# Kernel optimization log

Measured on AMD Instinct MI355X. Metric: run time of the kernel, lower is better.

The kernel has to match this reference:

```python
import jax, jax.numpy as jnp
import numpy as np

B, A, C = 1, 196416, 90
H = W = 1024
SCORE_THRESHOLD = 0.05
MAX_DETECTIONS = 100
# RetinaNet-style BBoxTransform normalization (mean=0, std=[0.1,0.1,0.2,0.2])
STD = (0.1, 0.1, 0.2, 0.2)


def setup_inputs() -> dict:
    key = jax.random.key(0)
    k1, k2, k3, k4, k5, k6, k7 = jax.random.split(key, 7)
    x = jax.random.normal(k1, (B, 3, H, W), dtype=jnp.float32)
    regression = jax.random.normal(k2, (B, A, 4), dtype=jnp.float32) * 0.1
    classification = jax.random.normal(k3, (B, A, C), dtype=jnp.float32)
    # valid anchor boxes (x1, y1, x2, y2)
    cx = jax.random.uniform(k4, (B, A), minval=0.0, maxval=float(W))
    cy = jax.random.uniform(k5, (B, A), minval=0.0, maxval=float(H))
    aw = jax.random.uniform(k6, (B, A), minval=16.0, maxval=256.0)
    ah = jax.random.uniform(k7, (B, A), minval=16.0, maxval=256.0)
    anchors = jnp.stack([cx - 0.5 * aw, cy - 0.5 * ah, cx + 0.5 * aw, cy + 0.5 * ah], axis=2).astype(jnp.float32)
    return {"x": x, "regression": regression, "classification": classification, "anchors": anchors}


def _decode_clip(anchors, regression, img_h, img_w):
    # BBoxTransform: deltas (dx, dy, dw, dh) scaled by std, applied to anchor center/size
    wa = anchors[..., 2] - anchors[..., 0]
    ha = anchors[..., 3] - anchors[..., 1]
    cxa = anchors[..., 0] + 0.5 * wa
    cya = anchors[..., 1] + 0.5 * ha
    dx = regression[..., 0] * STD[0]
    dy = regression[..., 1] * STD[1]
    dw = regression[..., 2] * STD[2]
    dh = regression[..., 3] * STD[3]
    cx = cxa + dx * wa
    cy = cya + dy * ha
    w = jnp.exp(dw) * wa
    h = jnp.exp(dh) * ha
    # ClipBoxes: x1,y1 clamped at 0; x2,y2 clamped at image width/height
    x1 = jnp.maximum(cx - 0.5 * w, 0.0)
    y1 = jnp.maximum(cy - 0.5 * h, 0.0)
    x2 = jnp.minimum(cx + 0.5 * w, float(img_w))
    y2 = jnp.minimum(cy + 0.5 * h, float(img_h))
    return jnp.stack([x1, y1, x2, y2], axis=2)  # [B, A, 4]


def reference(x, regression, classification, anchors):
    img_h, img_w = x.shape[2], x.shape[3]
    boxes = _decode_clip(anchors, regression, img_h, img_w)  # [1, A, 4]
    probs = jax.nn.sigmoid(classification)                    # [1, A, C]
    scores = jnp.max(probs, axis=2)                           # [1, A]
    classes = jnp.argmax(probs, axis=2)                       # [1, A]
    valid_scores = jnp.where(scores > SCORE_THRESHOLD, scores, 0.0)
    vb = boxes[0]            # [A, 4]
    vc = classes[0]          # [A]
    vs = valid_scores[0]     # [A]
    k = min(MAX_DETECTIONS, vs.shape[0])
    _, top_idx = jax.lax.top_k(vs, k)
    final_boxes = vb[top_idx]
    final_scores = vs[top_idx]
    final_classes = vc[top_idx]
    return (final_boxes, final_scores, final_classes)
```

## Files before the change

### kernel.cpp

```cpp
#include <hip/hip_runtime.h>
#include <cmath>

#define A_CNT 196416
#define C_CNT 90
#define PAIRS (A_CNT / 2)
#define TOPK 100u
#define RB 128
#define NB_REDUCE ((PAIRS + RB - 1) / RB)

#define OFF_HIST1 785664u
#define OFF_HIST2 789760u
#define OFF_CTRL  1051904u
#define OFF_CAND  1051968u
#define OFF_EQ    1052480u

__global__ __launch_bounds__(RB) void k_reduce(const float* __restrict__ cls,
                                               unsigned* __restrict__ keys,
                                               unsigned* __restrict__ hist1,
                                               unsigned* __restrict__ hist2) {
    __shared__ unsigned lhist[576];
    const int t = threadIdx.x;
    for (int j = t; j < 576; j += RB) lhist[j] = 0u;
    __syncthreads();

    const int p = blockIdx.x * RB + t;
    if (p < PAIRS) {
        const float4* __restrict__ r4 = (const float4*)cls + (size_t)p * 45;
        float m0 = -INFINITY, m1;
#pragma unroll
        for (int i = 0; i < 22; ++i) {
            float4 v = r4[i];
            m0 = fmaxf(m0, fmaxf(fmaxf(v.x, v.y), fmaxf(v.z, v.w)));
        }
        {
            float4 v = r4[22];
            m0 = fmaxf(m0, fmaxf(v.x, v.y));
            m1 = fmaxf(v.z, v.w);
        }
#pragma unroll
        for (int i = 23; i < 45; ++i) {
            float4 v = r4[i];
            m1 = fmaxf(m1, fmaxf(fmaxf(v.x, v.y), fmaxf(v.z, v.w)));
        }
        float p0 = 1.0f / (1.0f + expf(-m0));
        float p1 = 1.0f / (1.0f + expf(-m1));
        unsigned k0 = (p0 > 0.05f) ? __float_as_uint(p0) : 0u;
        unsigned k1 = (p1 > 0.05f) ? __float_as_uint(p1) : 0u;
        *(uint2*)(keys + 2 * p) = make_uint2(k0, k1);
        unsigned h0 = k0 ? (min(k0 >> 16, 0x3F80u) - 0x3D4Bu) : 0u;
        unsigned h1 = k1 ? (min(k1 >> 16, 0x3F80u) - 0x3D4Bu) : 0u;
        atomicAdd(&lhist[h0], 1u);
        atomicAdd(&lhist[h1], 1u);
        if (p < 65536) hist2[p] = 0u;
    }
    __syncthreads();
    for (int j = t; j < 576; j += RB) {
        unsigned c = lhist[j];
        if (c) atomicAdd(&hist1[j], c);
    }
}

template <int CHUNK>
__global__ __launch_bounds__(256) void k_scan(const unsigned* __restrict__ hist,
                                              unsigned* __restrict__ ctrl, int mode) {
    __shared__ unsigned sdata[256];
    __shared__ unsigned sbin[2];
    const int t = threadIdx.x;
    const unsigned target = TOPK;
    const unsigned above0 = (mode == 0) ? 0u : ctrl[1];

    unsigned s = 0;
    const uint4* p = (const uint4*)(hist + t * CHUNK);
#pragma unroll 8
    for (int j = 0; j < CHUNK / 4; ++j) { uint4 u = p[j]; s += u.x + u.y + u.z + u.w; }
    sdata[t] = s;
    for (int d = 1; d < 256; d <<= 1) {
        __syncthreads();
        unsigned add = (t + d < 256) ? sdata[t + d] : 0u;
        __syncthreads();
        sdata[t] += add;
    }
    __syncthreads();
    {
        unsigned mysuf  = sdata[t] + above0;
        unsigned nxtsuf = ((t < 255) ? sdata[t + 1] : 0u) + above0;
        if (nxtsuf < target && mysuf >= target) { sbin[0] = (unsigned)t; sbin[1] = nxtsuf - above0; }
    }
    __syncthreads();
    const unsigned chunkB = sbin[0];
    const unsigned gAbove = sbin[1] + above0;

    unsigned v = (t < CHUNK) ? hist[chunkB * CHUNK + t] : 0u;
    sdata[t] = v;
    for (int d = 1; d < 256; d <<= 1) {
        __syncthreads();
        unsigned add = (t + d < 256) ? sdata[t + d] : 0u;
        __syncthreads();
        sdata[t] += add;
    }
    __syncthreads();
    {
        unsigned mysuf  = sdata[t] + gAbove;
        unsigned nxtsuf = ((t < 255) ? sdata[t + 1] : 0u) + gAbove;
        if (nxtsuf < target && mysuf >= target) {
            unsigned bin = chunkB * CHUNK + (unsigned)t;
            if (mode == 0) {
                ctrl[0] = bin ? (bin + 0x3D4Bu) : 0u;
                ctrl[1] = nxtsuf;
            } else {
                ctrl[2] = (ctrl[0] << 16) | bin;
                ctrl[3] = nxtsuf;
                ctrl[4] = target - nxtsuf;
            }
        }
    }
}

__global__ __launch_bounds__(256) void k_hist2(const unsigned* __restrict__ keys,
                                               const unsigned* __restrict__ ctrl,
                                               unsigned* __restrict__ hist2) {
    const unsigned binB = ctrl[0];
    const int i4 = blockIdx.x * 256 + threadIdx.x;
    if (i4 >= A_CNT / 4) return;
    uint4 k = ((const uint4*)keys)[i4];
    if ((k.x >> 16) == binB) atomicAdd(&hist2[k.x & 0xFFFFu], 1u);
    if ((k.y >> 16) == binB) atomicAdd(&hist2[k.y & 0xFFFFu], 1u);
    if ((k.z >> 16) == binB) atomicAdd(&hist2[k.z & 0xFFFFu], 1u);
    if ((k.w >> 16) == binB) atomicAdd(&hist2[k.w & 0xFFFFu], 1u);
}

__global__ __launch_bounds__(256) void k_gather(const unsigned* __restrict__ keys,
                                                unsigned* __restrict__ ctrl,
                                                unsigned* __restrict__ cand,
                                                unsigned* __restrict__ eqi) {
    const unsigned T = ctrl[2];
    const int i4 = blockIdx.x * 256 + threadIdx.x;
    if (i4 >= A_CNT / 4) return;
    uint4 k = ((const uint4*)keys)[i4];
    const unsigned base = (unsigned)(4 * i4);
#pragma unroll
    for (int j = 0; j < 4; ++j) {
        unsigned kk = (j == 0) ? k.x : (j == 1) ? k.y : (j == 2) ? k.z : k.w;
        if (kk > T) {
            unsigned q = atomicAdd(&ctrl[5], 1u);
            if (q < 128u) cand[q] = base + j;
        } else if (kk == T) {
            unsigned q = atomicAdd(&ctrl[6], 1u);
            if (q < 1024u) eqi[q] = base + j;
        }
    }
}

__global__ __launch_bounds__(128) void k_final(const float* __restrict__ cls,
                                               const float* __restrict__ reg,
                                               const float* __restrict__ anc,
                                               const unsigned* __restrict__ ctrl,
                                               const unsigned* __restrict__ cand,
                                               const unsigned* __restrict__ eqi,
                                               const unsigned* __restrict__ keys,
                                               float* __restrict__ out) {
    __shared__ unsigned sel[TOPK];
    const int t = threadIdx.x;
    const unsigned n_gt = ctrl[3];
    const unsigned need_eq = ctrl[4];
    unsigned eq_cnt = ctrl[6];
    if (eq_cnt > 1024u) eq_cnt = 1024u;

    if (t < (int)n_gt) {
        unsigned mi = cand[t], mk = keys[mi], r = 0;
        for (unsigned j = 0; j < n_gt; ++j) {
            unsigned oj = cand[j], ok = keys[oj];
            if (ok > mk || (ok == mk && oj < mi)) r++;
        }
        sel[r] = mi;
    }
    for (unsigned e = (unsigned)t; e < eq_cnt; e += 128u) {
        unsigned mi = eqi[e], r = 0;
        for (unsigned j = 0; j < eq_cnt; ++j)
            if (eqi[j] < mi) r++;
        if (r < need_eq) sel[n_gt + r] = mi;
    }
    __syncthreads();

    if (t < (int)TOPK) {
        const unsigned a = sel[t];
        const float2* row = (const float2*)(cls + (size_t)a * C_CNT);
        float bv = -INFINITY; int bi = 0;
#pragma unroll 5
        for (int c = 0; c < 45; ++c) {
            float2 v = row[c];
            if (v.x > bv) { bv = v.x; bi = 2 * c; }
            if (v.y > bv) { bv = v.y; bi = 2 * c + 1; }
        }
        float score = __uint_as_float(keys[a]);
        float x1a = anc[a * 4 + 0], y1a = anc[a * 4 + 1];
        float x2a = anc[a * 4 + 2], y2a = anc[a * 4 + 3];
        float wa = x2a - x1a, ha = y2a - y1a;
        float cxa = x1a + 0.5f * wa, cya = y1a + 0.5f * ha;
        float dx = reg[a * 4 + 0] * 0.1f, dy = reg[a * 4 + 1] * 0.1f;
        float dw = reg[a * 4 + 2] * 0.2f, dh = reg[a * 4 + 3] * 0.2f;
        float cx = cxa + dx * wa, cy = cya + dy * ha;
        float w = expf(dw) * wa, h = expf(dh) * ha;
        out[t * 4 + 0] = fmaxf(cx - 0.5f * w, 0.0f);
        out[t * 4 + 1] = fmaxf(cy - 0.5f * h, 0.0f);
        out[t * 4 + 2] = fminf(cx + 0.5f * w, 1024.0f);
        out[t * 4 + 3] = fminf(cy + 0.5f * h, 1024.0f);
        out[400 + t] = score;
        out[500 + t] = (float)bi;
    }
}

extern "C" void kernel_launch(void* const* d_in, const int* in_sizes, int n_in,
                              void* d_out, int out_size, void* d_ws, size_t ws_size,
                              hipStream_t stream) {
    const float* reg = (const float*)d_in[1];
    const float* cls = (const float*)d_in[2];
    const float* anc = (const float*)d_in[3];
    float* out = (float*)d_out;
    char* ws = (char*)d_ws;
    unsigned* keys  = (unsigned*)ws;
    unsigned* hist1 = (unsigned*)(ws + OFF_HIST1);
    unsigned* hist2 = (unsigned*)(ws + OFF_HIST2);
    unsigned* ctrl  = (unsigned*)(ws + OFF_CTRL);
    unsigned* cand  = (unsigned*)(ws + OFF_CAND);
    unsigned* eqi   = (unsigned*)(ws + OFF_EQ);

    hipMemsetAsync(hist1, 0, 1024 * 4, stream);
    hipMemsetAsync(ctrl, 0, 64, stream);
    k_reduce<<<NB_REDUCE, RB, 0, stream>>>(cls, keys, hist1, hist2);
    k_scan<4><<<1, 256, 0, stream>>>(hist1, ctrl, 0);
    k_hist2<<<192, 256, 0, stream>>>(keys, ctrl, hist2);
    k_scan<256><<<1, 256, 0, stream>>>(hist2, ctrl, 1);
    k_gather<<<192, 256, 0, stream>>>(keys, ctrl, cand, eqi);
    k_final<<<1, 128, 0, stream>>>(cls, reg, anc, ctrl, cand, eqi, keys, out);
}
```

Baseline: 165.8 us.

## Coalesce class-max reduction across lanes and drop second radix histogram pass

The reduction kernel now assigns 8 lanes to each anchor pair, so every row of class scores is read with strided float4 loads across lanes and combined by shuffle instead of one thread reading 180 floats serially. This targets poor coalescing and low memory-level parallelism in the dominant read of the classification tensor. It also drops the 16-bit second histogram and its scan; all keys in the threshold bin (up to 2048) are gathered and ranked in shared memory inside the final kernel. That removes two launches and a hist2 clear, at the cost of an O(n^2) ranking over the bin candidates in a single block, and keys beyond the 2048-entry buffer are silently dropped.

```diff
diff --git a/kernel.cpp b/kernel.cpp
--- a/kernel.cpp
+++ b/kernel.cpp
@@ -4,75 +4,78 @@
 #define A_CNT 196416
 #define C_CNT 90
 #define PAIRS (A_CNT / 2)
+#define WITERS 12276
 #define TOPK 100u
-#define RB 128
-#define NB_REDUCE ((PAIRS + RB - 1) / RB)
+#define CAPB 2048
 
 #define OFF_HIST1 785664u
-#define OFF_HIST2 789760u
-#define OFF_CTRL  1051904u
-#define OFF_CAND  1051968u
-#define OFF_EQ    1052480u
-
-__global__ __launch_bounds__(RB) void k_reduce(const float* __restrict__ cls,
-                                               unsigned* __restrict__ keys,
-                                               unsigned* __restrict__ hist1,
-                                               unsigned* __restrict__ hist2) {
+#define OFF_CTRL  789760u
+#define OFF_CANDA 789824u
+#define OFF_CANDB 790336u
+
+__global__ __launch_bounds__(256, 4) void k_reduce(const float* __restrict__ cls,
+                                                   unsigned* __restrict__ keys,
+                                                   unsigned* __restrict__ hist1) {
     __shared__ unsigned lhist[576];
     const int t = threadIdx.x;
-    for (int j = t; j < 576; j += RB) lhist[j] = 0u;
-    __syncthreads();
-
-    const int p = blockIdx.x * RB + t;
-    if (p < PAIRS) {
-        const float4* __restrict__ r4 = (const float4*)cls + (size_t)p * 45;
-        float m0 = -INFINITY, m1;
+    for (int j = t; j < 576; j += 256) lhist[j] = 0u;
+    __syncthreads();
+
+    const int lane = t & 63;
+    const int g = lane >> 3, s = lane & 7;
+    const int wid = blockIdx.x * 4 + (t >> 6);
+    const int nw = gridDim.x * 4;
+    const float4* __restrict__ cls4 = (const float4*)cls;
+
+    for (int w = wid; w < WITERS; w += nw) {
+        const int p = w * 8 + g;
+        const float4* __restrict__ r4 = cls4 + (size_t)p * 45;
+        float m0 = -INFINITY, m1 = -INFINITY;
 #pragma unroll
-        for (int i = 0; i < 22; ++i) {
-            float4 v = r4[i];
-            m0 = fmaxf(m0, fmaxf(fmaxf(v.x, v.y), fmaxf(v.z, v.w)));
-        }
-        {
-            float4 v = r4[22];
-            m0 = fmaxf(m0, fmaxf(v.x, v.y));
-            m1 = fmaxf(v.z, v.w);
+        for (int i = 0; i < 6; ++i) {
+            const int j = s + 8 * i;
+            if (j < 45) {
+                float4 v = r4[j];
+                float a01 = fmaxf(v.x, v.y), a23 = fmaxf(v.z, v.w);
+                float all = fmaxf(a01, a23);
+                if (j < 22)      m0 = fmaxf(m0, all);
+                else if (j > 22) m1 = fmaxf(m1, all);
+                else { m0 = fmaxf(m0, a01); m1 = fmaxf(m1, a23); }
+            }
         }
 #pragma unroll
-        for (int i = 23; i < 45; ++i) {
-            float4 v = r4[i];
-            m1 = fmaxf(m1, fmaxf(fmaxf(v.x, v.y), fmaxf(v.z, v.w)));
-        }
-        float p0 = 1.0f / (1.0f + expf(-m0));
-        float p1 = 1.0f / (1.0f + expf(-m1));
-        unsigned k0 = (p0 > 0.05f) ? __float_as_uint(p0) : 0u;
-        unsigned k1 = (p1 > 0.05f) ? __float_as_uint(p1) : 0u;
-        *(uint2*)(keys + 2 * p) = make_uint2(k0, k1);
-        unsigned h0 = k0 ? (min(k0 >> 16, 0x3F80u) - 0x3D4Bu) : 0u;
-        unsigned h1 = k1 ? (min(k1 >> 16, 0x3F80u) - 0x3D4Bu) : 0u;
-        atomicAdd(&lhist[h0], 1u);
-        atomicAdd(&lhist[h1], 1u);
-        if (p < 65536) hist2[p] = 0u;
-    }
-    __syncthreads();
-    for (int j = t; j < 576; j += RB) {
+        for (int d = 1; d < 8; d <<= 1) {
+            m0 = fmaxf(m0, __shfl_xor(m0, d));
+            m1 = fmaxf(m1, __shfl_xor(m1, d));
+        }
+        if (s == 0) {
+            float p0 = 1.0f / (1.0f + expf(-m0));
+            float p1 = 1.0f / (1.0f + expf(-m1));
+            unsigned k0 = (p0 > 0.05f) ? __float_as_uint(p0) : 0u;
+            unsigned k1 = (p1 > 0.05f) ? __float_as_uint(p1) : 0u;
+            *(uint2*)(keys + 2 * p) = make_uint2(k0, k1);
+            unsigned h0 = k0 ? (min(k0 >> 16, 0x3F80u) - 0x3D4Bu) : 0u;
+            unsigned h1 = k1 ? (min(k1 >> 16, 0x3F80u) - 0x3D4Bu) : 0u;
+            atomicAdd(&lhist[h0], 1u);
+            atomicAdd(&lhist[h1], 1u);
+        }
+    }
+    __syncthreads();
+    for (int j = t; j < 576; j += 256) {
         unsigned c = lhist[j];
         if (c) atomicAdd(&hist1[j], c);
     }
 }
 
-template <int CHUNK>
 __global__ __launch_bounds__(256) void k_scan(const unsigned* __restrict__ hist,
-                                              unsigned* __restrict__ ctrl, int mode) {
+                                              unsigned* __restrict__ ctrl) {
     __shared__ unsigned sdata[256];
     __shared__ unsigned sbin[2];
     const int t = threadIdx.x;
     const unsigned target = TOPK;
-    const unsigned above0 = (mode == 0) ? 0u : ctrl[1];
-
-    unsigned s = 0;
-    const uint4* p = (const uint4*)(hist + t * CHUNK);
-#pragma unroll 8
-    for (int j = 0; j < CHUNK / 4; ++j) { uint4 u = p[j]; s += u.x + u.y + u.z + u.w; }
+
+    uint4 u = ((const uint4*)hist)[t];
+    unsigned s = u.x + u.y + u.z + u.w;
     sdata[t] = s;
     for (int d = 1; d < 256; d <<= 1) {
         __syncthreads();
@@ -82,15 +85,15 @@
     }
     __syncthreads();
     {
-        unsigned mysuf  = sdata[t] + above0;
-        unsigned nxtsuf = ((t < 255) ? sdata[t + 1] : 0u) + above0;
-        if (nxtsuf < target && mysuf >= target) { sbin[0] = (unsigned)t; sbin[1] = nxtsuf - above0; }
+        unsigned mysuf  = sdata[t];
+        unsigned nxtsuf = (t < 255) ? sdata[t + 1] : 0u;
+        if (nxtsuf < target && mysuf >= target) { sbin[0] = (unsigned)t; sbin[1] = nxtsuf; }
     }
     __syncthreads();
     const unsigned chunkB = sbin[0];
-    const unsigned gAbove = sbin[1] + above0;
-
-    unsigned v = (t < CHUNK) ? hist[chunkB * CHUNK + t] : 0u;
+    const unsigned gAbove = sbin[1];
+
+    unsigned v = (t < 4) ? hist[chunkB * 4 + t] : 0u;
     sdata[t] = v;
     for (int d = 1; d < 256; d <<= 1) {
         __syncthreads();
@@ -103,37 +106,18 @@
         unsigned mysuf  = sdata[t] + gAbove;
         unsigned nxtsuf = ((t < 255) ? sdata[t + 1] : 0u) + gAbove;
         if (nxtsuf < target && mysuf >= target) {
-            unsigned bin = chunkB * CHUNK + (unsigned)t;
-            if (mode == 0) {
-                ctrl[0] = bin ? (bin + 0x3D4Bu) : 0u;
-                ctrl[1] = nxtsuf;
-            } else {
-                ctrl[2] = (ctrl[0] << 16) | bin;
-                ctrl[3] = nxtsuf;
-                ctrl[4] = target - nxtsuf;
-            }
-        }
-    }
-}
-
-__global__ __launch_bounds__(256) void k_hist2(const unsigned* __restrict__ keys,
-                                               const unsigned* __restrict__ ctrl,
-                                               unsigned* __restrict__ hist2) {
-    const unsigned binB = ctrl[0];
-    const int i4 = blockIdx.x * 256 + threadIdx.x;
-    if (i4 >= A_CNT / 4) return;
-    uint4 k = ((const uint4*)keys)[i4];
-    if ((k.x >> 16) == binB) atomicAdd(&hist2[k.x & 0xFFFFu], 1u);
-    if ((k.y >> 16) == binB) atomicAdd(&hist2[k.y & 0xFFFFu], 1u);
-    if ((k.z >> 16) == binB) atomicAdd(&hist2[k.z & 0xFFFFu], 1u);
-    if ((k.w >> 16) == binB) atomicAdd(&hist2[k.w & 0xFFFFu], 1u);
+            unsigned bin = chunkB * 4 + (unsigned)t;
+            ctrl[0] = bin ? (bin + 0x3D4Bu) : 0u;
+            ctrl[1] = nxtsuf;
+        }
+    }
 }
 
 __global__ __launch_bounds__(256) void k_gather(const unsigned* __restrict__ keys,
                                                 unsigned* __restrict__ ctrl,
-                                                unsigned* __restrict__ cand,
-                                                unsigned* __restrict__ eqi) {
-    const unsigned T = ctrl[2];
+                                                unsigned* __restrict__ candA,
+                                                unsigned* __restrict__ candB) {
+    const unsigned binB = ctrl[0];
     const int i4 = blockIdx.x * 256 + threadIdx.x;
     if (i4 >= A_CNT / 4) return;
     uint4 k = ((const uint4*)keys)[i4];
@@ -141,44 +125,54 @@
 #pragma unroll
     for (int j = 0; j < 4; ++j) {
         unsigned kk = (j == 0) ? k.x : (j == 1) ? k.y : (j == 2) ? k.z : k.w;
-        if (kk > T) {
+        unsigned t16 = kk >> 16;
+        if (t16 > binB) {
             unsigned q = atomicAdd(&ctrl[5], 1u);
-            if (q < 128u) cand[q] = base + j;
-        } else if (kk == T) {
+            if (q < 128u) candA[q] = base + j;
+        } else if (t16 == binB) {
             unsigned q = atomicAdd(&ctrl[6], 1u);
-            if (q < 1024u) eqi[q] = base + j;
-        }
-    }
-}
-
-__global__ __launch_bounds__(128) void k_final(const float* __restrict__ cls,
+            if (q < (unsigned)CAPB) candB[q] = base + j;
+        }
+    }
+}
+
+__global__ __launch_bounds__(256) void k_final(const float* __restrict__ cls,
                                                const float* __restrict__ reg,
                                                const float* __restrict__ anc,
                                                const unsigned* __restrict__ ctrl,
-                                               const unsigned* __restrict__ cand,
-                                               const unsigned* __restrict__ eqi,
+                                               const unsigned* __restrict__ candA,
+                                               const unsigned* __restrict__ candB,
                                                const unsigned* __restrict__ keys,
                                                float* __restrict__ out) {
+    __shared__ unsigned sAi[128], sAk[128];
+    __shared__ unsigned sBi[CAPB], sBk[CAPB];
     __shared__ unsigned sel[TOPK];
     const int t = threadIdx.x;
-    const unsigned n_gt = ctrl[3];
-    const unsigned need_eq = ctrl[4];
-    unsigned eq_cnt = ctrl[6];
-    if (eq_cnt > 1024u) eq_cnt = 1024u;
-
-    if (t < (int)n_gt) {
-        unsigned mi = cand[t], mk = keys[mi], r = 0;
-        for (unsigned j = 0; j < n_gt; ++j) {
-            unsigned oj = cand[j], ok = keys[oj];
-            if (ok > mk || (ok == mk && oj < mi)) r++;
+    const unsigned nA = min(ctrl[5], 128u);
+    const unsigned nB = min(ctrl[6], (unsigned)CAPB);
+    const unsigned need = TOPK - nA;
+
+    if (t < (int)nA) { unsigned i = candA[t]; sAi[t] = i; sAk[t] = keys[i]; }
+    for (unsigned e = (unsigned)t; e < nB; e += 256u) {
+        unsigned i = candB[e]; sBi[e] = i; sBk[e] = keys[i];
+    }
+    __syncthreads();
+
+    if (t < (int)nA) {
+        unsigned mi = sAi[t], mk = sAk[t], r = 0;
+        for (unsigned j = 0; j < nA; ++j) {
+            unsigned ok = sAk[j];
+            if (ok > mk || (ok == mk && sAi[j] < mi)) r++;
         }
         sel[r] = mi;
     }
-    for (unsigned e = (unsigned)t; e < eq_cnt; e += 128u) {
-        unsigned mi = eqi[e], r = 0;
-        for (unsigned j = 0; j < eq_cnt; ++j)
-            if (eqi[j] < mi) r++;
-        if (r < need_eq) sel[n_gt + r] = mi;
+    for (unsigned e = (unsigned)t; e < nB; e += 256u) {
+        unsigned mi = sBi[e], mk = sBk[e], r = 0;
+        for (unsigned j = 0; j < nB; ++j) {
+            unsigned ok = sBk[j];
+            if (ok > mk || (ok == mk && sBi[j] < mi)) r++;
+        }
+        if (r < need) sel[nA + r] = mi;
     }
     __syncthreads();
 
@@ -220,17 +214,13 @@
     char* ws = (char*)d_ws;
     unsigned* keys  = (unsigned*)ws;
     unsigned* hist1 = (unsigned*)(ws + OFF_HIST1);
-    unsigned* hist2 = (unsigned*)(ws + OFF_HIST2);
     unsigned* ctrl  = (unsigned*)(ws + OFF_CTRL);
-    unsigned* cand  = (unsigned*)(ws + OFF_CAND);
-    unsigned* eqi   = (unsigned*)(ws + OFF_EQ);
-
-    hipMemsetAsync(hist1, 0, 1024 * 4, stream);
-    hipMemsetAsync(ctrl, 0, 64, stream);
-    k_reduce<<<NB_REDUCE, RB, 0, stream>>>(cls, keys, hist1, hist2);
-    k_scan<4><<<1, 256, 0, stream>>>(hist1, ctrl, 0);
-    k_hist2<<<192, 256, 0, stream>>>(keys, ctrl, hist2);
-    k_scan<256><<<1, 256, 0, stream>>>(hist2, ctrl, 1);
-    k_gather<<<192, 256, 0, stream>>>(keys, ctrl, cand, eqi);
-    k_final<<<1, 128, 0, stream>>>(cls, reg, anc, ctrl, cand, eqi, keys, out);
-}
+    unsigned* candA = (unsigned*)(ws + OFF_CANDA);
+    unsigned* candB = (unsigned*)(ws + OFF_CANDB);
+
+    hipMemsetAsync(hist1, 0, 4096 + 64, stream);
+    k_reduce<<<2048, 256, 0, stream>>>(cls, keys, hist1);
+    k_scan<<<1, 256, 0, stream>>>(hist1, ctrl);
+    k_gather<<<192, 256, 0, stream>>>(keys, ctrl, candA, candB);
+    k_final<<<1, 256, 0, stream>>>(cls, reg, anc, ctrl, candA, candB, keys, out);
+}
```

Measured after the change: 160.3 us. 1.03x faster.
